# Kernel tuning notes

Hardware: AMD Instinct MI355X
Metric: run time of the kernel (lower is better)

The kernel has to match this reference:

```python
import jax, jax.numpy as jnp
import numpy as np

N = 100000   # nodes per graph (50k users + 50k items)
E = 1600000  # edges per graph
D = 128      # feature / hidden dim
B = 100000   # train pairs per domain
NUM_USER = 50000
LAMBDA = 1.0


def setup_inputs() -> dict:
    key = jax.random.key(0)
    ks = jax.random.split(key, 24)
    s = 1.0 / np.sqrt(D)
    return {
        "feats_s": jax.random.normal(ks[0], (N, D), jnp.float32),
        "feats_t": jax.random.normal(ks[1], (N, D), jnp.float32),
        "W1": jax.random.normal(ks[2], (D, D), jnp.float32) * s,
        "b1": jnp.zeros((D,), jnp.float32),
        "W2": jax.random.normal(ks[3], (D, D), jnp.float32) * s,
        "b2": jnp.zeros((D,), jnp.float32),
        "cls_W": jax.random.normal(ks[4], (2 * D, 1), jnp.float32) * s,
        "cls_b": jnp.zeros((1,), jnp.float32),
        "du_W": jax.random.normal(ks[5], (D, 1), jnp.float32) * s,
        "du_b": jnp.zeros((1,), jnp.float32),
        "di_W": jax.random.normal(ks[6], (D, 1), jnp.float32) * s,
        "di_b": jnp.zeros((1,), jnp.float32),
        "edge_src_s": jax.random.randint(ks[7], (E,), 0, N, jnp.int32),
        "edge_dst_s": jax.random.randint(ks[8], (E,), 0, N, jnp.int32),
        "edge_src_t": jax.random.randint(ks[9], (E,), 0, N, jnp.int32),
        "edge_dst_t": jax.random.randint(ks[10], (E,), 0, N, jnp.int32),
        "user_s": jax.random.randint(ks[11], (B,), 0, NUM_USER, jnp.int32),
        "item_s": jax.random.randint(ks[12], (B,), 0, NUM_USER, jnp.int32),
        "labels_s": jax.random.randint(ks[13], (B,), 0, 2, jnp.int32),
        "user_t": jax.random.randint(ks[14], (B,), 0, NUM_USER, jnp.int32),
        "item_t": jax.random.randint(ks[15], (B,), 0, NUM_USER, jnp.int32),
        "labels_t": jax.random.randint(ks[16], (B,), 0, 2, jnp.int32),
        "num_user_ds": NUM_USER,
        "num_user_dt": NUM_USER,
    }


def _gcn_layer(x, W, b, src, dst, dinv):
    # PyG GCNConv: out[i] = sum_{j->i} dinv[j]*dinv[i] * (x @ W)[j] + b
    h = x @ W
    norm = (dinv[src] * dinv[dst])[:, None]
    return jax.ops.segment_sum(h[src] * norm, dst, num_segments=x.shape[0]) + b


def _encode(x, src, dst, W1, b1, W2, b2):
    n = x.shape[0]
    sl = jnp.arange(n, dtype=src.dtype)            # self loops
    src = jnp.concatenate([src, sl])
    dst = jnp.concatenate([dst, sl])
    deg = jax.ops.segment_sum(jnp.ones_like(dst, dtype=x.dtype), dst, num_segments=n)
    dinv = jax.lax.rsqrt(jnp.maximum(deg, 1.0))    # deg >= 1 due to self loops
    h = jax.nn.relu(_gcn_layer(x, W1, b1, src, dst, dinv))
    return _gcn_layer(h, W2, b2, src, dst, dinv)   # dropout is identity at eval


def _bce_from_logits(z, y):
    # mean BCE on sigmoid(z), numerically stable
    return jnp.mean(y * jax.nn.softplus(-z) + (1.0 - y) * jax.nn.softplus(z))


def reference(feats_s, feats_t, W1, b1, W2, b2, cls_W, cls_b, du_W, du_b, di_W, di_b,
              edge_src_s, edge_dst_s, edge_src_t, edge_dst_t,
              user_s, item_s, labels_s, user_t, item_t, labels_t,
              num_user_ds, num_user_dt):
    x_ds = _encode(feats_s, edge_src_s, edge_dst_s, W1, b1, W2, b2)
    x_dt = _encode(feats_t, edge_src_t, edge_dst_t, W1, b1, W2, b2)

    ufs = x_ds[user_s]
    ifs = x_ds[item_s + num_user_ds]
    uft = x_dt[user_t]
    ift = x_dt[item_t + num_user_dt]

    z_s = (jnp.concatenate([ufs, ifs], axis=1) @ cls_W).reshape(-1) + cls_b[0]
    z_t = (jnp.concatenate([uft, ift], axis=1) @ cls_W).reshape(-1) + cls_b[0]
    clf_loss = _bce_from_logits(z_s, labels_s.astype(jnp.float32)) + \
               _bce_from_logits(z_t, labels_t.astype(jnp.float32))

    cu_s = jax.nn.sigmoid((ufs @ du_W).reshape(-1) + du_b[0])
    cu_t = jax.nn.sigmoid((uft @ du_W).reshape(-1) + du_b[0])
    ci_s = jax.nn.sigmoid((ifs @ di_W).reshape(-1) + di_b[0])
    ci_t = jax.nn.sigmoid((ift @ di_W).reshape(-1) + di_b[0])
    domain_loss = jnp.abs(jnp.mean(cu_s) - jnp.mean(cu_t)) + \
                  jnp.abs(jnp.mean(ci_s) - jnp.mean(ci_t))

    return clf_loss + LAMBDA * domain_loss
```

## Files before the change

### kernel.cpp

```cpp
#include <hip/hip_runtime.h>

#define D 128
#define NB 512
#define BSLACK 4160
#define CHUNK 8

typedef __attribute__((ext_vector_type(8))) short bf16x8;
typedef __attribute__((ext_vector_type(4))) float f32x4;
typedef __attribute__((ext_vector_type(2))) float f32x2;
typedef __attribute__((ext_vector_type(4))) int i32x4;

static __device__ inline unsigned pack_bf16x2(float a, float b) {
    unsigned ua = __float_as_uint(a);
    unsigned ub = __float_as_uint(b);
    ua += 0x7fffu + ((ua >> 16) & 1u);
    ub += 0x7fffu + ((ub >> 16) & 1u);
    return (ua >> 16) | (ub & 0xffff0000u);
}

__global__ __launch_bounds__(256) void bh_k(const int* __restrict__ dst_s,
                                            const int* __restrict__ dst_t,
                                            int* __restrict__ bcnt, int E) {
    int d = blockIdx.y;
    const int* dst = d ? dst_t : dst_s;
    __shared__ int h[NB];
    for (int i = threadIdx.x; i < NB; i += 256) h[i] = 0;
    __syncthreads();
    int stride = gridDim.x * 256;
    for (int e = blockIdx.x * 256 + threadIdx.x; e < E; e += stride)
        atomicAdd(&h[dst[e] >> 8], 1);
    __syncthreads();
    for (int i = threadIdx.x; i < NB; i += 256)
        if (h[i]) atomicAdd(&bcnt[d * NB + i], h[i]);
}

__global__ __launch_bounds__(1024) void scanB_k(const int* __restrict__ bcnt,
                                                int* __restrict__ bbase,
                                                int* __restrict__ cursor) {
    __shared__ int sh[1024];
    int t = threadIdx.x;
    int v = bcnt[t];
    sh[t] = v;
    __syncthreads();
    for (int o = 1; o < 1024; o <<= 1) {
        int x = (t >= o) ? sh[t - o] : 0;
        __syncthreads();
        sh[t] += x;
        __syncthreads();
    }
    int ex = sh[t] - v;
    bbase[t] = ex; cursor[t] = ex;
    if (t == 1023) bbase[1024] = sh[1023];
}

__global__ __launch_bounds__(256) void bin_k(const int* __restrict__ src_s,
                                             const int* __restrict__ dst_s,
                                             const int* __restrict__ src_t,
                                             const int* __restrict__ dst_t,
                                             int* __restrict__ cursor,
                                             unsigned* __restrict__ pairs, int E) {
    int d = blockIdx.y;
    const int* src = d ? src_t : src_s;
    const int* dst = d ? dst_t : dst_s;
    int* cur = cursor + d * NB;
    __shared__ int h[NB];
    __shared__ int gb[NB];
    int t0 = blockIdx.x * 2048;
    if (t0 >= E) return;
    for (int i = threadIdx.x; i < NB; i += 256) h[i] = 0;
    __syncthreads();
    int rank[8]; unsigned pk[8]; short bk[8];
    #pragma unroll
    for (int j = 0; j < 8; ++j) {
        int e = t0 + j * 256 + threadIdx.x;
        if (e < E) {
            int dd = dst[e], s = src[e];
            bk[j] = (short)(dd >> 8);
            pk[j] = (unsigned)s | ((unsigned)(dd & 255) << 24);
            rank[j] = atomicAdd(&h[dd >> 8], 1);
        } else bk[j] = -1;
    }
    __syncthreads();
    for (int i = threadIdx.x; i < NB; i += 256)
        gb[i] = h[i] ? atomicAdd(&cur[i], h[i]) : 0;
    __syncthreads();
    #pragma unroll
    for (int j = 0; j < 8; ++j)
        if (bk[j] >= 0) pairs[gb[bk[j]] + rank[j]] = pk[j];
}

__global__ __launch_bounds__(256) void csrb_k(const unsigned* __restrict__ pairs,
                                              const int* __restrict__ bbase,
                                              int2* __restrict__ nspan,
                                              float* __restrict__ dinv,
                                              int* __restrict__ csr, int N) {
    int d = blockIdx.y, bx = blockIdx.x, t = threadIdx.x;
    int g = d * NB + bx;
    int e0 = bbase[g], e1 = bbase[g + 1];
    int cbase = ((e0 + 15) & ~15) + g * BSLACK;
    float* dv = dinv + (size_t)d * (N + 1);
    int2* ns = nspan + (size_t)d * N;
    __shared__ int lh[256];
    __shared__ int lex[256];
    __shared__ int lc[256];
    lh[t] = 0; lc[t] = 0;
    __syncthreads();
    for (int e = e0 + t; e < e1; e += 256)
        atomicAdd(&lh[pairs[e] >> 24], 1);
    __syncthreads();
    int node = (bx << 8) + t;
    bool valid = node < N;
    int deg = lh[t];
    int pdeg = valid ? (((deg + 16) >> 4) << 4) : 0;
    lex[t] = pdeg;
    __syncthreads();
    for (int o = 1; o < 256; o <<= 1) {
        int x = (t >= o) ? lex[t - o] : 0;
        __syncthreads();
        lex[t] += x;
        __syncthreads();
    }
    int start = cbase + lex[t] - pdeg;
    if (valid) {
        ns[node] = make_int2(start, start + pdeg);
        dv[node] = rsqrtf((float)(deg + 1));
    }
    lex[t] = start;
    __syncthreads();
    for (int e = e0 + t; e < e1; e += 256) {
        unsigned p = pairs[e];
        int dn = p >> 24;
        int rank = atomicAdd(&lc[dn], 1);
        csr[lex[dn] + rank] = (int)(p & 0xffffffu);
    }
    __syncthreads();
    if (valid) {
        int b = lex[t];
        csr[b + deg] = node;
        for (int k = deg + 1; k < pdeg; ++k) csr[b + k] = N;
    }
    if (t == 255) {
        int bend = start + pdeg;
        for (int i = 0; i < 48; ++i) csr[bend + i] = N;
    }
    if (bx == 0 && t == 0) dv[N] = 0.f;
}

__global__ __launch_bounds__(256) void packW_k(const float* __restrict__ W1,
                                               const float* __restrict__ W2,
                                               unsigned short* __restrict__ wp1,
                                               unsigned short* __restrict__ wp2) {
    const float* W = blockIdx.x ? W2 : W1;
    unsigned short* wp = blockIdx.x ? wp2 : wp1;
    for (int idx = threadIdx.x; idx < 2048; idx += 256) {
        int f = idx >> 6, lane = idx & 63;
        int t = f >> 2, c = f & 3;
        int q = lane >> 4, nn = lane & 15;
        #pragma unroll
        for (int j = 0; j < 8; ++j) {
            unsigned u = __float_as_uint(W[(c * 32 + q * 8 + j) * 128 + t * 16 + nn]);
            u += 0x7fffu + ((u >> 16) & 1u);
            wp[idx * 8 + j] = (unsigned short)(u >> 16);
        }
    }
}

__global__ __launch_bounds__(256) void gemm_mfma(const void* __restrict__ xs,
                                                 const void* __restrict__ xt,
                                                 const unsigned short* __restrict__ wp,
                                                 unsigned* __restrict__ hb,
                                                 const float* __restrict__ dinv,
                                                 int N, int in_bf16) {
    int d = blockIdx.y;
    const void* xin = d ? xt : xs;
    unsigned* out = hb + (size_t)d * (N + 1) * 32;
    const float* dv = dinv + (size_t)d * (N + 1);
    __shared__ float cs[64 * 132];
    int tid = threadIdx.x;
    int wave = tid >> 6, lane = tid & 63;
    int quad = lane >> 4, nn = lane & 15;
    long long blockbase = (long long)blockIdx.x * 64;
    long long ar = blockbase + wave * 16 + nn;
    if (ar > N - 1) ar = N - 1;

    bf16x8 a[4];
    if (in_bf16) {
        const uint4* xr = (const uint4*)((const unsigned short*)xin + ar * 128);
        #pragma unroll
        for (int c = 0; c < 4; ++c) {
            union { uint4 u; bf16x8 v; } cv;
            cv.u = xr[c * 4 + quad];
            a[c] = cv.v;
        }
    } else {
        const float4* xr = (const float4*)((const float*)xin + ar * 128);
        #pragma unroll
        for (int c = 0; c < 4; ++c) {
            float4 lo = xr[c * 8 + quad * 2];
            float4 hi = xr[c * 8 + quad * 2 + 1];
            union { bf16x8 v; unsigned u[4]; } au;
            au.u[0] = pack_bf16x2(lo.x, lo.y);
            au.u[1] = pack_bf16x2(lo.z, lo.w);
            au.u[2] = pack_bf16x2(hi.x, hi.y);
            au.u[3] = pack_bf16x2(hi.z, hi.w);
            a[c] = au.v;
        }
    }

    f32x4 acc[8];
    #pragma unroll
    for (int t = 0; t < 8; ++t) acc[t] = (f32x4){0.f, 0.f, 0.f, 0.f};
    const bf16x8* wf = (const bf16x8*)wp;
    #pragma unroll
    for (int t = 0; t < 8; ++t) {
        #pragma unroll
        for (int c = 0; c < 4; ++c) {
            bf16x8 b = wf[(t * 4 + c) * 64 + lane];
            acc[t] = __builtin_amdgcn_mfma_f32_16x16x32_bf16(a[c], b, acc[t], 0, 0, 0);
        }
    }

    #pragma unroll
    for (int t = 0; t < 8; ++t) {
        #pragma unroll
        for (int r = 0; r < 4; ++r)
            cs[(wave * 16 + quad * 4 + r) * 132 + t * 16 + nn] = acc[t][r];
    }
    __syncthreads();

    #pragma unroll
    for (int i = 0; i < 8; ++i) {
        int idx = tid + i * 256;
        int r = idx >> 5, c4 = idx & 31;
        long long row = blockbase + r;
        if (row <= N) {
            float s = dv[row];
            const float4 v = *(const float4*)&cs[r * 132 + c4 * 4];
            int pk = __builtin_amdgcn_cvt_pk_fp8_f32(v.x * s, v.y * s, 0, false);
            pk = __builtin_amdgcn_cvt_pk_fp8_f32(v.z * s, v.w * s, pk, true);
            out[row * 32 + c4] = (unsigned)pk;
        }
    }
}

#define NTLD(p) __builtin_nontemporal_load((const i32x4*)(p))
#define SBAR __builtin_amdgcn_sched_barrier(0);

#define AGG_GATHER(u, q0, q1)                                                \
        u[0] = hsl[((unsigned)(q0).x) << 5];                                 \
        u[1] = hsl[((unsigned)(q0).y) << 5];                                 \
        u[2] = hsl[((unsigned)(q0).z) << 5];                                 \
        u[3] = hsl[((unsigned)(q0).w) << 5];                                 \
        u[4] = hsl[((unsigned)(q1).x) << 5];                                 \
        u[5] = hsl[((unsigned)(q1).y) << 5];                                 \
        u[6] = hsl[((unsigned)(q1).z) << 5];                                 \
        u[7] = hsl[((unsigned)(q1).w) << 5];

#define AGG_CONSUME(u)                                                       \
        { f32x2 lo, hi;                                                      \
          lo = __builtin_amdgcn_cvt_pk_f32_fp8((int)u[0], false);            \
          hi = __builtin_amdgcn_cvt_pk_f32_fp8((int)u[0], true);             \
          s01 += lo; s23 += hi;                                              \
          lo = __builtin_amdgcn_cvt_pk_f32_fp8((int)u[1], false);            \
          hi = __builtin_amdgcn_cvt_pk_f32_fp8((int)u[1], true);             \
          s01 += lo; s23 += hi;                                              \
          lo = __builtin_amdgcn_cvt_pk_f32_fp8((int)u[2], false);            \
          hi = __builtin_amdgcn_cvt_pk_f32_fp8((int)u[2], true);             \
          s01 += lo; s23 += hi;                                              \
          lo = __builtin_amdgcn_cvt_pk_f32_fp8((int)u[3], false);            \
          hi = __builtin_amdgcn_cvt_pk_f32_fp8((int)u[3], true);             \
          s01 += lo; s23 += hi;                                              \
          lo = __builtin_amdgcn_cvt_pk_f32_fp8((int)u[4], false);            \
          hi = __builtin_amdgcn_cvt_pk_f32_fp8((int)u[4], true);             \
          s01 += lo; s23 += hi;                                              \
          lo = __builtin_amdgcn_cvt_pk_f32_fp8((int)u[5], false);            \
          hi = __builtin_amdgcn_cvt_pk_f32_fp8((int)u[5], true);             \
          s01 += lo; s23 += hi;                                              \
          lo = __builtin_amdgcn_cvt_pk_f32_fp8((int)u[6], false);            \
          hi = __builtin_amdgcn_cvt_pk_f32_fp8((int)u[6], true);             \
          s01 += lo; s23 += hi;                                              \
          lo = __builtin_amdgcn_cvt_pk_f32_fp8((int)u[7], false);            \
          hi = __builtin_amdgcn_cvt_pk_f32_fp8((int)u[7], true);             \
          s01 += lo; s23 += hi; }

#define BOUND                                                                \
        if (en >= end) {                                                     \
            finalize(k);                                                     \
            if (++k >= cnt) break;                                           \
            end = __shfl(myns.y, k);                                         \
            s01 = (f32x2){0.f, 0.f};                                         \
            s23 = (f32x2){0.f, 0.f};                                         \
        }                                                                    \
        e = en;

#define AGG_PIPE_LOOP                                                        \
    i32x4 a0 = NTLD(cp + e), a1 = NTLD(cp + e + 4);                          \
    i32x4 b0 = NTLD(cp + e + 16), b1 = NTLD(cp + e + 20);                    \
    i32x4 t0 = NTLD(cp + e + 32), t1 = NTLD(cp + e + 36);                    \
    unsigned uA[8], uB[8], uC[8];                                            \
    AGG_GATHER(uA, a0, a1)                                                   \
    AGG_GATHER(uB, b0, b1)                                                   \
    SBAR                                                                     \
    for (;;) {                                                               \
        int en = e + 16;                                                     \
        AGG_GATHER(uC, t0, t1)                                               \
        a0 = NTLD(cp + e + 48); a1 = NTLD(cp + e + 52);                      \
        SBAR                                                                 \
        AGG_CONSUME(uA)                                                      \
        BOUND                                                                \
        en = e + 16;                                                         \
        AGG_GATHER(uA, a0, a1)                                               \
        b0 = NTLD(cp + e + 48); b1 = NTLD(cp + e + 52);                      \
        SBAR                                                                 \
        AGG_CONSUME(uB)                                                      \
        BOUND                                                                \
        en = e + 16;                                                         \
        AGG_GATHER(uB, b0, b1)                                               \
        t0 = NTLD(cp + e + 48); t1 = NTLD(cp + e + 52);                      \
        SBAR                                                                 \
        AGG_CONSUME(uC)                                                      \
        BOUND                                                                \
    }

__global__ __launch_bounds__(256, 4) void agg1_k(const unsigned* __restrict__ hb,
                                                 const float* __restrict__ dinv,
                                                 const int2* __restrict__ nspan,
                                                 const int* __restrict__ csr,
                                                 const float* __restrict__ bias,
                                                 uint2* __restrict__ out, int N) {
    int d = blockIdx.y;
    const unsigned* hs = hb + (size_t)d * (N + 1) * 32;
    const float* dv = dinv + (size_t)d * (N + 1);
    const int2* ns = nspan + (size_t)d * N;
    uint2* outp = out + (size_t)d * N * 32;
    int wave = threadIdx.x >> 6, lane = threadIdx.x & 63;
    int node0 = (blockIdx.x * 4 + wave) * CHUNK;
    if (node0 >= N) return;
    int cnt = min(CHUNK, N - node0);
    int half = lane >> 5, li = lane & 31;
    int lc = lane & (CHUNK - 1);
    int2 myns = make_int2(0, 0);
    float mydv = 0.f;
    if (lc < cnt) { myns = ns[node0 + lc]; mydv = dv[node0 + lc]; }
    float4 b4 = ((const float4*)bias)[li];
    const unsigned* hsl = hs + li;
    const int* cp = csr + 8 * half;

    f32x2 s01 = (f32x2){0.f, 0.f};
    f32x2 s23 = (f32x2){0.f, 0.f};

    auto finalize = [&](int kk) {
        float a0f = s01[0], a1f = s01[1], a2f = s23[0], a3f = s23[1];
        a0f += __shfl_xor(a0f, 32);
        a1f += __shfl_xor(a1f, 32);
        a2f += __shfl_xor(a2f, 32);
        a3f += __shfl_xor(a3f, 32);
        float dik = __shfl(mydv, kk);
        float o0 = fmaxf(fmaf(dik, a0f, b4.x), 0.f);
        float o1 = fmaxf(fmaf(dik, a1f, b4.y), 0.f);
        float o2 = fmaxf(fmaf(dik, a2f, b4.z), 0.f);
        float o3 = fmaxf(fmaf(dik, a3f, b4.w), 0.f);
        if (half == 0)
            outp[(size_t)(node0 + kk) * 32 + li] =
                make_uint2(pack_bf16x2(o0, o1), pack_bf16x2(o2, o3));
    };

    int k = 0;
    int e = __shfl(myns.x, 0);
    int end = __shfl(myns.y, 0);
    AGG_PIPE_LOOP
}

__global__ __launch_bounds__(256, 4) void agg2_k(const unsigned* __restrict__ hb,
                                                 const float* __restrict__ dinv,
                                                 const int2* __restrict__ nspan,
                                                 const int* __restrict__ csr,
                                                 const float* __restrict__ bias,
                                                 const float* __restrict__ clsW,
                                                 const float* __restrict__ duW,
                                                 const float* __restrict__ diW,
                                                 const int* __restrict__ nus,
                                                 const int* __restrict__ nut,
                                                 float2* __restrict__ nodeDots, int N) {
    int d = blockIdx.y;
    const unsigned* hs = hb + (size_t)d * (N + 1) * 32;
    const float* dv = dinv + (size_t)d * (N + 1);
    const int2* ns = nspan + (size_t)d * N;
    float2* nd = nodeDots + (size_t)d * N;
    int nu = d ? nut[0] : nus[0];
    int wave = threadIdx.x >> 6, lane = threadIdx.x & 63;
    int node0 = (blockIdx.x * 4 + wave) * CHUNK;
    if (node0 >= N) return;
    int cnt = min(CHUNK, N - node0);
    int half = lane >> 5, li = lane & 31;
    int lc = lane & (CHUNK - 1);
    int2 myns = make_int2(0, 0);
    float mydv = 0.f;
    if (lc < cnt) { myns = ns[node0 + lc]; mydv = dv[node0 + lc]; }
    float4 b4 = ((const float4*)bias)[li];
    float4 wA0 = ((const float4*)clsW)[li];
    float4 wA1 = ((const float4*)clsW)[32 + li];
    float4 wB0 = ((const float4*)duW)[li];
    float4 wB1 = ((const float4*)diW)[li];
    const unsigned* hsl = hs + li;
    const int* cp = csr + 8 * half;

    f32x2 s01 = (f32x2){0.f, 0.f};
    f32x2 s23 = (f32x2){0.f, 0.f};

    auto finalize = [&](int kk) {
        float a0f = s01[0], a1f = s01[1], a2f = s23[0], a3f = s23[1];
        a0f += __shfl_xor(a0f, 32);
        a1f += __shfl_xor(a1f, 32);
        a2f += __shfl_xor(a2f, 32);
        a3f += __shfl_xor(a3f, 32);
        float dik = __shfl(mydv, kk);
        float o0 = fmaf(dik, a0f, b4.x);
        float o1 = fmaf(dik, a1f, b4.y);
        float o2 = fmaf(dik, a2f, b4.z);
        float o3 = fmaf(dik, a3f, b4.w);
        int nodek = node0 + kk;
        int sel = (nodek >= nu) ? 1 : 0;
        float4 wA = sel ? wA1 : wA0;
        float4 wB = sel ? wB1 : wB0;
        float p = o0 * wA.x + o1 * wA.y + o2 * wA.z + o3 * wA.w;
        float q = o0 * wB.x + o1 * wB.y + o2 * wB.z + o3 * wB.w;
        #pragma unroll
        for (int o = 16; o > 0; o >>= 1) {
            p += __shfl_xor(p, o);
            q += __shfl_xor(q, o);
        }
        if (lane == 0) nd[nodek] = make_float2(p, q);
    };

    int k = 0;
    int e = __shfl(myns.x, 0);
    int end = __shfl(myns.y, 0);
    AGG_PIPE_LOOP
}

__global__ __launch_bounds__(256) void loss_k(const float2* __restrict__ nodeDots,
                                              const int* __restrict__ us, const int* __restrict__ is_,
                                              const int* __restrict__ ls,
                                              const int* __restrict__ ut, const int* __restrict__ it,
                                              const int* __restrict__ lt,
                                              const float* __restrict__ clsb,
                                              const float* __restrict__ dub,
                                              const float* __restrict__ dib,
                                              const int* __restrict__ nus,
                                              const int* __restrict__ nut,
                                              float* __restrict__ accum, int Bn, int N) {
    int d = blockIdx.y;
    const float2* nd = nodeDots + (size_t)d * N;
    const int* users = d ? ut : us;
    const int* items = d ? it : is_;
    const int* labels = d ? lt : ls;
    int nu = d ? nut[0] : nus[0];
    float* acc = accum + 3 * d;
    int k = blockIdx.x * 256 + threadIdx.x;
    float bce = 0.f, cu = 0.f, ci = 0.f;
    if (k < Bn) {
        int u = users[k];
        int t = items[k] + nu;
        float2 ud = nd[u];
        float2 id = nd[t];
        float z = ud.x + id.x + clsb[0];
        float y = (float)labels[k];
        float sp = fmaxf(z, 0.f) + log1pf(expf(-fabsf(z)));
        bce = sp - y * z;
        cu = 1.f / (1.f + expf(-(ud.y + dub[0])));
        ci = 1.f / (1.f + expf(-(id.y + dib[0])));
    }
    #pragma unroll
    for (int o = 32; o > 0; o >>= 1) {
        bce += __shfl_xor(bce, o);
        cu += __shfl_xor(cu, o);
        ci += __shfl_xor(ci, o);
    }
    __shared__ float sh[12];
    int lane = threadIdx.x & 63, wave = threadIdx.x >> 6;
    if (lane == 0) { sh[wave * 3 + 0] = bce; sh[wave * 3 + 1] = cu; sh[wave * 3 + 2] = ci; }
    __syncthreads();
    if (threadIdx.x < 3) {
        float v = sh[threadIdx.x] + sh[3 + threadIdx.x] + sh[6 + threadIdx.x] + sh[9 + threadIdx.x];
        atomicAdd(&acc[threadIdx.x], v);
    }
}

__global__ void finalize_k(const float* __restrict__ accum, float* __restrict__ out, float invB) {
    if (threadIdx.x == 0 && blockIdx.x == 0) {
        float clf = (accum[0] + accum[3]) * invB;
        float dom = fabsf((accum[1] - accum[4]) * invB) + fabsf((accum[2] - accum[5]) * invB);
        out[0] = clf + dom;
    }
}

extern "C" void kernel_launch(void* const* d_in, const int* in_sizes, int n_in,
                              void* d_out, int out_size, void* d_ws, size_t ws_size,
                              hipStream_t stream) {
    const float* feats_s = (const float*)d_in[0];
    const float* feats_t = (const float*)d_in[1];
    const float* W1   = (const float*)d_in[2];
    const float* b1   = (const float*)d_in[3];
    const float* W2   = (const float*)d_in[4];
    const float* b2   = (const float*)d_in[5];
    const float* clsW = (const float*)d_in[6];
    const float* clsb = (const float*)d_in[7];
    const float* duW  = (const float*)d_in[8];
    const float* dub  = (const float*)d_in[9];
    const float* diW  = (const float*)d_in[10];
    const float* dib  = (const float*)d_in[11];

    int N = in_sizes[0] / D;
    int E = in_sizes[12];
    int B = in_sizes[16];
    int nb = (N + 255) >> 8;

    char* ws = (char*)d_ws;
    size_t off = 0;
    auto alloc = [&](size_t bytes) -> void* {
        void* p = ws + off;
        off += (bytes + 255) & ~(size_t)255;
        return p;
    };
    int*      bcnt   = (int*)  alloc(2 * NB * 4);
    int*      bbase  = (int*)  alloc((2 * NB + 1) * 4);
    int*      cursor = (int*)  alloc(2 * NB * 4);
    float*    dinv   = (float*)alloc((size_t)2 * (N + 1) * 4);
    int2*     nspan  = (int2*) alloc((size_t)2 * N * 8);
    unsigned* pairs  = (unsigned*)alloc((size_t)2 * E * 4);
    int*      csr    = (int*)  alloc(((size_t)2 * E + 2 * NB * BSLACK + 256) * 4);
    unsigned* hbuf8  = (unsigned*)alloc((size_t)2 * (N + 1) * 128);
    unsigned* abuf   = (unsigned*)alloc((size_t)2 * N * 256);
    float2*   nodeDots = (float2*)alloc((size_t)2 * N * 8);
    unsigned short* wp1 = (unsigned short*)alloc(16384 * 2);
    unsigned short* wp2 = (unsigned short*)alloc(16384 * 2);
    float*    accum  = (float*)alloc(128);

    hipMemsetAsync(accum, 0, 6 * sizeof(float), stream);
    hipMemsetAsync(bcnt, 0, 2 * NB * 4, stream);

    const int* esrc_s = (const int*)d_in[12];
    const int* edst_s = (const int*)d_in[13];
    const int* esrc_t = (const int*)d_in[14];
    const int* edst_t = (const int*)d_in[15];
    const int* user_s = (const int*)d_in[16];
    const int* item_s = (const int*)d_in[17];
    const int* lab_s  = (const int*)d_in[18];
    const int* user_t = (const int*)d_in[19];
    const int* item_t = (const int*)d_in[20];
    const int* lab_t  = (const int*)d_in[21];
    const int* nup_s  = (const int*)d_in[22];
    const int* nup_t  = (const int*)d_in[23];

    packW_k<<<2, 256, 0, stream>>>(W1, W2, wp1, wp2);

    bh_k<<<dim3(512, 2), 256, 0, stream>>>(edst_s, edst_t, bcnt, E);
    scanB_k<<<1, 1024, 0, stream>>>(bcnt, bbase, cursor);
    bin_k<<<dim3((E + 2047) / 2048, 2), 256, 0, stream>>>(esrc_s, edst_s, esrc_t, edst_t,
                                                          cursor, pairs, E);
    csrb_k<<<dim3(nb, 2), 256, 0, stream>>>(pairs, bbase, nspan, dinv, csr, N);

    int ngb = (N + 64) / 64;
    int nchunk = (N + CHUNK - 1) / CHUNK;
    gemm_mfma<<<dim3(ngb, 2), 256, 0, stream>>>(feats_s, feats_t, wp1, hbuf8, dinv, N, 0);
    agg1_k<<<dim3((nchunk + 3) / 4, 2), 256, 0, stream>>>(hbuf8, dinv, nspan, csr, b1,
                                                          (uint2*)abuf, N);
    gemm_mfma<<<dim3(ngb, 2), 256, 0, stream>>>(abuf, abuf + (size_t)N * 64, wp2,
                                                hbuf8, dinv, N, 1);
    agg2_k<<<dim3((nchunk + 3) / 4, 2), 256, 0, stream>>>(hbuf8, dinv, nspan, csr, b2,
                                                          clsW, duW, diW, nup_s, nup_t,
                                                          nodeDots, N);
    loss_k<<<dim3((B + 255) / 256, 2), 256, 0, stream>>>(nodeDots,
                                                         user_s, item_s, lab_s,
                                                         user_t, item_t, lab_t,
                                                         clsb, dub, dib, nup_s, nup_t,
                                                         accum, B, N);
    finalize_k<<<1, 64, 0, stream>>>(accum, (float*)d_out, 1.0f / (float)B);
}
```

Before: 490.7 us.

## Fold weight packing into scan, stage CSR in LDS, simplify aggregation pipeline

Moves the W1/W2 bf16 packing into the single-block scan kernel, which removes one kernel launch. The CSR build now assembles each bucket's neighbour lists in a 48KB LDS buffer and writes them out contiguously, keeping the old scattered global-write path as a fallback for large buckets. The aggregation loop goes from a 3-deep to a 2-deep register pipeline, drops the sched_barriers, and removes the occupancy hint of 4 from launch_bounds. The aggregation changes cut register pressure but also reduce latency hiding in the gather-bound kernels, and the large LDS allocation lowers csrb_k occupancy.

Measured after the change: 466.5 us. 4.9% less time.

```diff
diff --git a/kernel.cpp b/kernel.cpp
--- a/kernel.cpp
+++ b/kernel.cpp
@@ -4,6 +4,7 @@
 #define NB 512
 #define BSLACK 4160
 #define CHUNK 8
+#define LDSCAP 12288
 
 typedef __attribute__((ext_vector_type(8))) short bf16x8;
 typedef __attribute__((ext_vector_type(4))) float f32x4;
@@ -36,7 +37,11 @@
 
 __global__ __launch_bounds__(1024) void scanB_k(const int* __restrict__ bcnt,
                                                 int* __restrict__ bbase,
-                                                int* __restrict__ cursor) {
+                                                int* __restrict__ cursor,
+                                                const float* __restrict__ W1,
+                                                const float* __restrict__ W2,
+                                                unsigned short* __restrict__ wp1,
+                                                unsigned short* __restrict__ wp2) {
     __shared__ int sh[1024];
     int t = threadIdx.x;
     int v = bcnt[t];
@@ -51,6 +56,22 @@
     int ex = sh[t] - v;
     bbase[t] = ex; cursor[t] = ex;
     if (t == 1023) bbase[1024] = sh[1023];
+    #pragma unroll
+    for (int m = 0; m < 2; ++m) {
+        const float* W = m ? W2 : W1;
+        unsigned short* wp = m ? wp2 : wp1;
+        for (int idx = t; idx < 2048; idx += 1024) {
+            int f = idx >> 6, lane = idx & 63;
+            int tt = f >> 2, c = f & 3;
+            int q = lane >> 4, nn = lane & 15;
+            #pragma unroll
+            for (int j = 0; j < 8; ++j) {
+                unsigned u = __float_as_uint(W[(c * 32 + q * 8 + j) * 128 + tt * 16 + nn]);
+                u += 0x7fffu + ((u >> 16) & 1u);
+                wp[idx * 8 + j] = (unsigned short)(u >> 16);
+            }
+        }
+    }
 }
 
 __global__ __launch_bounds__(256) void bin_k(const int* __restrict__ src_s,
@@ -103,6 +124,7 @@
     __shared__ int lh[256];
     __shared__ int lex[256];
     __shared__ int lc[256];
+    __shared__ int ls[LDSCAP];
     lh[t] = 0; lc[t] = 0;
     __syncthreads();
     for (int e = e0 + t; e < e1; e += 256)
@@ -120,49 +142,53 @@
         lex[t] += x;
         __syncthreads();
     }
-    int start = cbase + lex[t] - pdeg;
+    int tot = lex[255];
+    int start_local = lex[t] - pdeg;
+    int start = cbase + start_local;
     if (valid) {
         ns[node] = make_int2(start, start + pdeg);
         dv[node] = rsqrtf((float)(deg + 1));
     }
-    lex[t] = start;
-    __syncthreads();
-    for (int e = e0 + t; e < e1; e += 256) {
-        unsigned p = pairs[e];
-        int dn = p >> 24;
-        int rank = atomicAdd(&lc[dn], 1);
-        csr[lex[dn] + rank] = (int)(p & 0xffffffu);
-    }
-    __syncthreads();
-    if (valid) {
-        int b = lex[t];
-        csr[b + deg] = node;
-        for (int k = deg + 1; k < pdeg; ++k) csr[b + k] = N;
-    }
-    if (t == 255) {
-        int bend = start + pdeg;
-        for (int i = 0; i < 48; ++i) csr[bend + i] = N;
+    bool fits = (tot + 48) <= LDSCAP;
+    __syncthreads();
+    lex[t] = fits ? start_local : start;
+    __syncthreads();
+    if (fits) {
+        for (int e = e0 + t; e < e1; e += 256) {
+            unsigned p = pairs[e];
+            int dn = p >> 24;
+            int r = atomicAdd(&lc[dn], 1);
+            ls[lex[dn] + r] = (int)(p & 0xffffffu);
+        }
+        __syncthreads();
+        if (valid) {
+            int b = lex[t];
+            ls[b + deg] = node;
+            for (int k = deg + 1; k < pdeg; ++k) ls[b + k] = N;
+        }
+        if (t < 48) ls[tot + t] = N;
+        __syncthreads();
+        int tt = tot + 48;
+        for (int i = t; i < tt; i += 256) csr[cbase + i] = ls[i];
+    } else {
+        for (int e = e0 + t; e < e1; e += 256) {
+            unsigned p = pairs[e];
+            int dn = p >> 24;
+            int r = atomicAdd(&lc[dn], 1);
+            csr[lex[dn] + r] = (int)(p & 0xffffffu);
+        }
+        __syncthreads();
+        if (valid) {
+            int b = lex[t];
+            csr[b + deg] = node;
+            for (int k = deg + 1; k < pdeg; ++k) csr[b + k] = N;
+        }
+        if (t == 255) {
+            int bend = start + pdeg;
+            for (int i = 0; i < 48; ++i) csr[bend + i] = N;
+        }
     }
     if (bx == 0 && t == 0) dv[N] = 0.f;
-}
-
-__global__ __launch_bounds__(256) void packW_k(const float* __restrict__ W1,
-                                               const float* __restrict__ W2,
-                                               unsigned short* __restrict__ wp1,
-                                               unsigned short* __restrict__ wp2) {
-    const float* W = blockIdx.x ? W2 : W1;
-    unsigned short* wp = blockIdx.x ? wp2 : wp1;
-    for (int idx = threadIdx.x; idx < 2048; idx += 256) {
-        int f = idx >> 6, lane = idx & 63;
-        int t = f >> 2, c = f & 3;
-        int q = lane >> 4, nn = lane & 15;
-        #pragma unroll
-        for (int j = 0; j < 8; ++j) {
-            unsigned u = __float_as_uint(W[(c * 32 + q * 8 + j) * 128 + t * 16 + nn]);
-            u += 0x7fffu + ((u >> 16) & 1u);
-            wp[idx * 8 + j] = (unsigned short)(u >> 16);
-        }
-    }
 }
 
 __global__ __launch_bounds__(256) void gemm_mfma(const void* __restrict__ xs,
@@ -244,7 +270,6 @@
 }
 
 #define NTLD(p) __builtin_nontemporal_load((const i32x4*)(p))
-#define SBAR __builtin_amdgcn_sched_barrier(0);
 
 #define AGG_GATHER(u, q0, q1)                                                \
         u[0] = hsl[((unsigned)(q0).x) << 5];                                 \
@@ -294,40 +319,29 @@
         e = en;
 
 #define AGG_PIPE_LOOP                                                        \
-    i32x4 a0 = NTLD(cp + e), a1 = NTLD(cp + e + 4);                          \
-    i32x4 b0 = NTLD(cp + e + 16), b1 = NTLD(cp + e + 20);                    \
-    i32x4 t0 = NTLD(cp + e + 32), t1 = NTLD(cp + e + 36);                    \
-    unsigned uA[8], uB[8], uC[8];                                            \
-    AGG_GATHER(uA, a0, a1)                                                   \
-    AGG_GATHER(uB, b0, b1)                                                   \
-    SBAR                                                                     \
+    i32x4 c0 = NTLD(cp + e), c1 = NTLD(cp + e + 4);                          \
+    unsigned uA[8], uB[8];                                                   \
+    AGG_GATHER(uA, c0, c1)                                                   \
+    c0 = NTLD(cp + e + 16); c1 = NTLD(cp + e + 20);                          \
     for (;;) {                                                               \
         int en = e + 16;                                                     \
-        AGG_GATHER(uC, t0, t1)                                               \
-        a0 = NTLD(cp + e + 48); a1 = NTLD(cp + e + 52);                      \
-        SBAR                                                                 \
+        AGG_GATHER(uB, c0, c1)                                               \
+        c0 = NTLD(cp + en + 16); c1 = NTLD(cp + en + 20);                    \
         AGG_CONSUME(uA)                                                      \
         BOUND                                                                \
         en = e + 16;                                                         \
-        AGG_GATHER(uA, a0, a1)                                               \
-        b0 = NTLD(cp + e + 48); b1 = NTLD(cp + e + 52);                      \
-        SBAR                                                                 \
+        AGG_GATHER(uA, c0, c1)                                               \
+        c0 = NTLD(cp + en + 16); c1 = NTLD(cp + en + 20);                    \
         AGG_CONSUME(uB)                                                      \
         BOUND                                                                \
-        en = e + 16;                                                         \
-        AGG_GATHER(uB, b0, b1)                                               \
-        t0 = NTLD(cp + e + 48); t1 = NTLD(cp + e + 52);                      \
-        SBAR                                                                 \
-        AGG_CONSUME(uC)                                                      \
-        BOUND                                                                \
-    }
-
-__global__ __launch_bounds__(256, 4) void agg1_k(const unsigned* __restrict__ hb,
-                                                 const float* __restrict__ dinv,
-                                                 const int2* __restrict__ nspan,
-                                                 const int* __restrict__ csr,
-                                                 const float* __restrict__ bias,
-                                                 uint2* __restrict__ out, int N) {
+    }
+
+__global__ __launch_bounds__(256) void agg1_k(const unsigned* __restrict__ hb,
+                                              const float* __restrict__ dinv,
+                                              const int2* __restrict__ nspan,
+                                              const int* __restrict__ csr,
+                                              const float* __restrict__ bias,
+                                              uint2* __restrict__ out, int N) {
     int d = blockIdx.y;
     const unsigned* hs = hb + (size_t)d * (N + 1) * 32;
     const float* dv = dinv + (size_t)d * (N + 1);
@@ -371,17 +385,17 @@
     AGG_PIPE_LOOP
 }
 
-__global__ __launch_bounds__(256, 4) void agg2_k(const unsigned* __restrict__ hb,
-                                                 const float* __restrict__ dinv,
-                                                 const int2* __restrict__ nspan,
-                                                 const int* __restrict__ csr,
-                                                 const float* __restrict__ bias,
-                                                 const float* __restrict__ clsW,
-                                                 const float* __restrict__ duW,
-                                                 const float* __restrict__ diW,
-                                                 const int* __restrict__ nus,
-                                                 const int* __restrict__ nut,
-                                                 float2* __restrict__ nodeDots, int N) {
+__global__ __launch_bounds__(256) void agg2_k(const unsigned* __restrict__ hb,
+                                              const float* __restrict__ dinv,
+                                              const int2* __restrict__ nspan,
+                                              const int* __restrict__ csr,
+                                              const float* __restrict__ bias,
+                                              const float* __restrict__ clsW,
+                                              const float* __restrict__ duW,
+                                              const float* __restrict__ diW,
+                                              const int* __restrict__ nus,
+                                              const int* __restrict__ nut,
+                                              float2* __restrict__ nodeDots, int N) {
     int d = blockIdx.y;
     const unsigned* hs = hb + (size_t)d * (N + 1) * 32;
     const float* dv = dinv + (size_t)d * (N + 1);
@@ -553,10 +567,8 @@
     const int* nup_s  = (const int*)d_in[22];
     const int* nup_t  = (const int*)d_in[23];
 
-    packW_k<<<2, 256, 0, stream>>>(W1, W2, wp1, wp2);
-
     bh_k<<<dim3(512, 2), 256, 0, stream>>>(edst_s, edst_t, bcnt, E);
-    scanB_k<<<1, 1024, 0, stream>>>(bcnt, bbase, cursor);
+    scanB_k<<<1, 1024, 0, stream>>>(bcnt, bbase, cursor, W1, W2, wp1, wp2);
     bin_k<<<dim3((E + 2047) / 2048, 2), 256, 0, stream>>>(esrc_s, edst_s, esrc_t, edst_t,
                                                           cursor, pairs, E);
     csrb_k<<<dim3(nb, 2), 256, 0, stream>>>(pairs, bbase, nspan, dinv, csr, N);
```
